# Kernel optimization log

Hardware: AMD Instinct MI355X
Metric: run time of the kernel (lower is better)

Reference implementation:

```python
import jax, jax.numpy as jnp
import numpy as np

B, IN_DIM, HID, N_WIRES = 8192, 2048, 2048, 8


def setup_inputs() -> dict:
    key = jax.random.key(0)
    ks = jax.random.split(key, 12)
    fan_in = IN_DIM + HID
    w_scale = 1.0 / np.sqrt(fan_in)  # ~ nn.Linear default init scale
    mk_w = lambda k: jax.random.normal(k, (N_WIRES, fan_in), jnp.float32) * w_scale
    mk_b = lambda k: jax.random.normal(k, (N_WIRES,), jnp.float32) * w_scale
    return {
        "x": jax.random.normal(ks[0], (B, IN_DIM), jnp.float32),
        "hx": jax.random.normal(ks[1], (B, HID), jnp.float32),
        "cx": jax.random.normal(ks[2], (B, HID), jnp.float32),
        "Wf": mk_w(ks[3]), "bf": mk_b(ks[4]),
        "Wi": mk_w(ks[5]), "bi": mk_b(ks[6]),
        "Wg": mk_w(ks[7]), "bg": mk_b(ks[8]),
        "Wo": mk_w(ks[9]), "bo": mk_b(ks[10]),
    }


def reference(x, hx, cx, Wf, bf, Wi, bi, Wg, bg, Wo, bo):
    combined = jnp.concatenate([x, hx], axis=1)  # [B, IN+HID]
    # Exact expectation of the RX-only circuit: E[#zeros - #ones] = sum_i cos(angle_i)
    q_exp = lambda W, b: jnp.sum(jnp.cos(combined @ W.T + b))
    f = jax.nn.sigmoid(q_exp(Wf, bf))
    i = jax.nn.sigmoid(q_exp(Wi, bi))
    g = jnp.tanh(q_exp(Wg, bg))
    o = jax.nn.sigmoid(q_exp(Wo, bo))
    cx_new = f * cx + i * g
    hx_new = o * jnp.tanh(cx_new)
    return hx_new, cx_new
```

## Files before the change

### kernel.cpp

```cpp
#include <hip/hip_runtime.h>
#include <hip/hip_bf16.h>
#include <cstdint>
#include <cstddef>

#define B_ROWS 8192
#define KDIM   4096
#define IN_DIM 2048
#define HIDDEN 2048
#define NJ     32
#define BK     64
#define SUBT   (KDIM / BK)
#define MROWS  16
#define TPB1   64
#define NBUF   4
#define GRID1  (B_ROWS / MROWS)

typedef __bf16 bf16x8 __attribute__((ext_vector_type(8)));
typedef float  f32x4  __attribute__((ext_vector_type(4)));

__device__ __forceinline__ bf16x8 cvt8(f32x4 a, f32x4 b) {
    bf16x8 r;
    r[0] = (__bf16)a.x; r[1] = (__bf16)a.y; r[2] = (__bf16)a.z; r[3] = (__bf16)a.w;
    r[4] = (__bf16)b.x; r[5] = (__bf16)b.y; r[6] = (__bf16)b.z; r[7] = (__bf16)b.w;
    return r;
}

__device__ __forceinline__ void gload_lds16(const void* g, void* lds) {
    __builtin_amdgcn_global_load_lds(
        (const __attribute__((address_space(1))) void*)g,
        (__attribute__((address_space(3))) void*)lds, 16, 0, 0);
}

extern "C" __global__ __launch_bounds__(TPB1)
void p1_full(const float* __restrict__ x,  const float* __restrict__ hx,
             const float* __restrict__ Wf, const float* __restrict__ Wi,
             const float* __restrict__ Wg, const float* __restrict__ Wo,
             const float* __restrict__ bfp, const float* __restrict__ bip,
             const float* __restrict__ bgp, const float* __restrict__ bop,
             float* __restrict__ qpart)
{
    __shared__ float Abuf[NBUF][MROWS * BK];
    __shared__ float Bbuf[NBUF][NJ * BK];

    const int lane = threadIdx.x & 63;
    const int lrow = lane & 15;
    const int rowblk = blockIdx.x * MROWS;

    const float* Ax = x  + (size_t)rowblk * IN_DIM;
    const float* Ah = hx + (size_t)rowblk * HIDDEN;

    int aOff[4];
#pragma unroll
    for (int p = 0; p < 4; ++p) {
        const int r  = p * 4 + (lane >> 4);
        const int cs = (lane & 15) ^ (r & 7);
        aOff[p] = r * 2048 + cs * 4;
    }
    const float* Wsrc[8] = {Wf, Wf, Wi, Wi, Wg, Wg, Wo, Wo};
    int bOffp[8];
#pragma unroll
    for (int sl = 0; sl < 8; ++sl) {
        const int j  = sl * 4 + (lane >> 4);
        const int j7 = j & 7;
        bOffp[sl] = j7 * KDIM + (((lane & 15) ^ j7) * 4);
    }

    int offA0[2], offA1[2], offB00[2], offB01[2], offB10[2], offB11[2];
#pragma unroll
    for (int st = 0; st < 2; ++st) {
        const int cu = st * 8 + (lane >> 4) * 2;
        offA0[st]  = lrow * 256 + (((cu + 0) ^ (lane & 7)) * 16);
        offA1[st]  = lrow * 256 + (((cu + 1) ^ (lane & 7)) * 16);
        offB00[st] = lrow * 256        + (((cu + 0) ^ (lane & 7)) * 16);
        offB01[st] = lrow * 256        + (((cu + 1) ^ (lane & 7)) * 16);
        offB10[st] = (lrow + 16) * 256 + (((cu + 0) ^ (lane & 7)) * 16);
        offB11[st] = (lrow + 16) * 256 + (((cu + 1) ^ (lane & 7)) * 16);
    }

    f32x4 acc0 = {0.f, 0.f, 0.f, 0.f};
    f32x4 acc1 = {0.f, 0.f, 0.f, 0.f};

    auto issue = [&](int s) {
        const int b = s & (NBUF - 1);
        const float* As = (s < SUBT / 2) ? (Ax + s * BK)
                                         : (Ah + (s - SUBT / 2) * BK);
#pragma unroll
        for (int p = 0; p < 4; ++p)
            gload_lds16(As + aOff[p], (char*)&Abuf[b][0] + p * 1024);
#pragma unroll
        for (int sl = 0; sl < 8; ++sl)
            gload_lds16(Wsrc[sl] + bOffp[sl] + s * BK,
                        (char*)&Bbuf[b][0] + sl * 1024);
    };
    auto compute = [&](int s) {
        const int b = s & (NBUF - 1);
        const char* Ab = (const char*)&Abuf[b][0];
        const char* Bb = (const char*)&Bbuf[b][0];
#pragma unroll
        for (int st = 0; st < 2; ++st) {
            f32x4 a0  = *reinterpret_cast<const f32x4*>(Ab + offA0[st]);
            f32x4 a1  = *reinterpret_cast<const f32x4*>(Ab + offA1[st]);
            f32x4 w00 = *reinterpret_cast<const f32x4*>(Bb + offB00[st]);
            f32x4 w01 = *reinterpret_cast<const f32x4*>(Bb + offB01[st]);
            f32x4 w10 = *reinterpret_cast<const f32x4*>(Bb + offB10[st]);
            f32x4 w11 = *reinterpret_cast<const f32x4*>(Bb + offB11[st]);
            bf16x8 af  = cvt8(a0, a1);
            bf16x8 bf0 = cvt8(w00, w01);
            bf16x8 bf1 = cvt8(w10, w11);
            acc0 = __builtin_amdgcn_mfma_f32_16x16x32_bf16(af, bf0, acc0, 0, 0, 0);
            acc1 = __builtin_amdgcn_mfma_f32_16x16x32_bf16(af, bf1, acc1, 0, 0, 0);
        }
    };

    issue(0);
    issue(1);
    issue(2);
#pragma unroll 4
    for (int s = 0; s < SUBT; ++s) {
        if (s + 3 < SUBT) issue(s + 3);
        if (s < SUBT - 3)
            asm volatile("s_waitcnt vmcnt(36)" ::: "memory");
        else if (s == SUBT - 3)
            asm volatile("s_waitcnt vmcnt(24)" ::: "memory");
        else if (s == SUBT - 2)
            asm volatile("s_waitcnt vmcnt(12)" ::: "memory");
        else
            asm volatile("s_waitcnt vmcnt(0)" ::: "memory");
        __builtin_amdgcn_sched_barrier(0);
        compute(s);
    }

    const float b0v = ((lrow & 8) ? bip : bfp)[lrow & 7];
    const float b1v = ((lrow & 8) ? bop : bgp)[lrow & 7];
    float v0 = 0.f, v1 = 0.f;
#pragma unroll
    for (int r = 0; r < 4; ++r) {
        v0 += cosf(acc0[r] + b0v);
        v1 += cosf(acc1[r] + b1v);
    }
    v0 += __shfl_xor(v0, 1, 64);  v1 += __shfl_xor(v1, 1, 64);
    v0 += __shfl_xor(v0, 2, 64);  v1 += __shfl_xor(v1, 2, 64);
    v0 += __shfl_xor(v0, 4, 64);  v1 += __shfl_xor(v1, 4, 64);
    v0 += __shfl_xor(v0, 16, 64); v1 += __shfl_xor(v1, 16, 64);
    v0 += __shfl_xor(v0, 32, 64); v1 += __shfl_xor(v1, 32, 64);
    if ((lane & 55) == 0) {
        const int gg = (lane >> 3) & 1;
        qpart[blockIdx.x * 4 + gg]     = v0;
        qpart[blockIdx.x * 4 + gg + 2] = v1;
    }
}

extern "C" __global__ __launch_bounds__(256)
void p3_elementwise(const float* __restrict__ cx, const float* __restrict__ qpart,
                    float* __restrict__ out)
{
    __shared__ float qs[4][4];
    const int tid  = threadIdx.x;
    const int wave = tid >> 6;
    const int lane = tid & 63;

    const f32x4* qp4 = (const f32x4*)qpart;
    f32x4 qa = qp4[tid];
    f32x4 qb = qp4[tid + 256];
    f32x4 qp = {qa.x + qb.x, qa.y + qb.y, qa.z + qb.z, qa.w + qb.w};
#pragma unroll
    for (int m = 1; m <= 32; m <<= 1) {
        qp.x += __shfl_xor(qp.x, m, 64);
        qp.y += __shfl_xor(qp.y, m, 64);
        qp.z += __shfl_xor(qp.z, m, 64);
        qp.w += __shfl_xor(qp.w, m, 64);
    }
    if (lane == 0) {
        qs[wave][0] = qp.x; qs[wave][1] = qp.y;
        qs[wave][2] = qp.z; qs[wave][3] = qp.w;
    }
    __syncthreads();
    const float qf = qs[0][0] + qs[1][0] + qs[2][0] + qs[3][0];
    const float qi = qs[0][1] + qs[1][1] + qs[2][1] + qs[3][1];
    const float qg = qs[0][2] + qs[1][2] + qs[2][2] + qs[3][2];
    const float qo = qs[0][3] + qs[1][3] + qs[2][3] + qs[3][3];

    const float f  = 1.f / (1.f + expf(-qf));
    const float ii = 1.f / (1.f + expf(-qi));
    const float g  = tanhf(qg);
    const float o  = 1.f / (1.f + expf(-qo));
    const float ig = ii * g;

    const size_t N  = (size_t)B_ROWS * HIDDEN;
    const size_t N4 = N >> 2;
    const f32x4* cx4 = (const f32x4*)cx;
    f32x4* outh = (f32x4*)out;
    f32x4* outc = (f32x4*)(out + N);

    for (size_t idx = (size_t)blockIdx.x * blockDim.x + tid; idx < N4;
         idx += (size_t)gridDim.x * blockDim.x) {
        f32x4 c = cx4[idx];
        f32x4 cn, hn;
        cn.x = fmaf(f, c.x, ig);
        cn.y = fmaf(f, c.y, ig);
        cn.z = fmaf(f, c.z, ig);
        cn.w = fmaf(f, c.w, ig);
        hn.x = o * tanhf(cn.x);
        hn.y = o * tanhf(cn.y);
        hn.z = o * tanhf(cn.z);
        hn.w = o * tanhf(cn.w);
        __builtin_nontemporal_store(cn, outc + idx);
        __builtin_nontemporal_store(hn, outh + idx);
    }
}

extern "C" void kernel_launch(void* const* d_in, const int* in_sizes, int n_in,
                              void* d_out, int out_size, void* d_ws, size_t ws_size,
                              hipStream_t stream)
{
    const float* x  = (const float*)d_in[0];
    const float* hx = (const float*)d_in[1];
    const float* cx = (const float*)d_in[2];
    const float* Wf = (const float*)d_in[3];
    const float* bf = (const float*)d_in[4];
    const float* Wi = (const float*)d_in[5];
    const float* bi = (const float*)d_in[6];
    const float* Wg = (const float*)d_in[7];
    const float* bg = (const float*)d_in[8];
    const float* Wo = (const float*)d_in[9];
    const float* bo = (const float*)d_in[10];
    float* out = (float*)d_out;

    float* qpart = (float*)d_ws;

    p1_full<<<dim3(GRID1), dim3(TPB1), 0, stream>>>(
        x, hx, Wf, Wi, Wg, Wo, bf, bi, bg, bo, qpart);
    p3_elementwise<<<dim3(2048), dim3(256), 0, stream>>>(cx, qpart, out);
}
```

Measured before the change: 64.93 us.

## Split K across two waves per block with LDS reduction of accumulators

```diff
diff --git a/kernel.cpp b/kernel.cpp
--- a/kernel.cpp
+++ b/kernel.cpp
@@ -9,10 +9,11 @@
 #define HIDDEN 2048
 #define NJ     32
 #define BK     64
-#define SUBT   (KDIM / BK)
+#define KHALF  2048
+#define SUBT   (KHALF / BK)
 #define MROWS  16
-#define TPB1   64
-#define NBUF   4
+#define TPB1   128
+#define NBUF   3
 #define GRID1  (B_ROWS / MROWS)
 
 typedef __bf16 bf16x8 __attribute__((ext_vector_type(8)));
@@ -39,15 +40,19 @@
              const float* __restrict__ bgp, const float* __restrict__ bop,
              float* __restrict__ qpart)
 {
-    __shared__ float Abuf[NBUF][MROWS * BK];
-    __shared__ float Bbuf[NBUF][NJ * BK];
-
-    const int lane = threadIdx.x & 63;
+    __shared__ float Abuf[2][NBUF][MROWS * BK];
+    __shared__ float Bbuf[2][NBUF][NJ * BK];
+
+    const int tid  = threadIdx.x;
+    const int wave = tid >> 6;
+    const int lane = tid & 63;
     const int lrow = lane & 15;
     const int rowblk = blockIdx.x * MROWS;
 
-    const float* Ax = x  + (size_t)rowblk * IN_DIM;
-    const float* Ah = hx + (size_t)rowblk * HIDDEN;
+    const float* Aglob = (wave == 0)
+        ? (x  + (size_t)rowblk * IN_DIM)
+        : (hx + (size_t)rowblk * HIDDEN);
+    const int kw = wave * KHALF;
 
     int aOff[4];
 #pragma unroll
@@ -81,21 +86,20 @@
     f32x4 acc1 = {0.f, 0.f, 0.f, 0.f};
 
     auto issue = [&](int s) {
-        const int b = s & (NBUF - 1);
-        const float* As = (s < SUBT / 2) ? (Ax + s * BK)
-                                         : (Ah + (s - SUBT / 2) * BK);
+        const int b = s % NBUF;
 #pragma unroll
         for (int p = 0; p < 4; ++p)
-            gload_lds16(As + aOff[p], (char*)&Abuf[b][0] + p * 1024);
+            gload_lds16(Aglob + aOff[p] + s * BK,
+                        (char*)&Abuf[wave][b][0] + p * 1024);
 #pragma unroll
         for (int sl = 0; sl < 8; ++sl)
-            gload_lds16(Wsrc[sl] + bOffp[sl] + s * BK,
-                        (char*)&Bbuf[b][0] + sl * 1024);
+            gload_lds16(Wsrc[sl] + bOffp[sl] + kw + s * BK,
+                        (char*)&Bbuf[wave][b][0] + sl * 1024);
     };
     auto compute = [&](int s) {
-        const int b = s & (NBUF - 1);
-        const char* Ab = (const char*)&Abuf[b][0];
-        const char* Bb = (const char*)&Bbuf[b][0];
+        const int b = s % NBUF;
+        const char* Ab = (const char*)&Abuf[wave][b][0];
+        const char* Bb = (const char*)&Bbuf[wave][b][0];
 #pragma unroll
         for (int st = 0; st < 2; ++st) {
             f32x4 a0  = *reinterpret_cast<const f32x4*>(Ab + offA0[st]);
@@ -114,39 +118,50 @@
 
     issue(0);
     issue(1);
-    issue(2);
-#pragma unroll 4
-    for (int s = 0; s < SUBT; ++s) {
-        if (s + 3 < SUBT) issue(s + 3);
-        if (s < SUBT - 3)
-            asm volatile("s_waitcnt vmcnt(36)" ::: "memory");
-        else if (s == SUBT - 3)
-            asm volatile("s_waitcnt vmcnt(24)" ::: "memory");
-        else if (s == SUBT - 2)
-            asm volatile("s_waitcnt vmcnt(12)" ::: "memory");
-        else
-            asm volatile("s_waitcnt vmcnt(0)" ::: "memory");
+    for (int s = 0; s < SUBT - 2; ++s) {
+        issue(s + 2);
+        asm volatile("s_waitcnt vmcnt(24)" ::: "memory");
         __builtin_amdgcn_sched_barrier(0);
         compute(s);
     }
-
-    const float b0v = ((lrow & 8) ? bip : bfp)[lrow & 7];
-    const float b1v = ((lrow & 8) ? bop : bgp)[lrow & 7];
-    float v0 = 0.f, v1 = 0.f;
-#pragma unroll
-    for (int r = 0; r < 4; ++r) {
-        v0 += cosf(acc0[r] + b0v);
-        v1 += cosf(acc1[r] + b1v);
-    }
-    v0 += __shfl_xor(v0, 1, 64);  v1 += __shfl_xor(v1, 1, 64);
-    v0 += __shfl_xor(v0, 2, 64);  v1 += __shfl_xor(v1, 2, 64);
-    v0 += __shfl_xor(v0, 4, 64);  v1 += __shfl_xor(v1, 4, 64);
-    v0 += __shfl_xor(v0, 16, 64); v1 += __shfl_xor(v1, 16, 64);
-    v0 += __shfl_xor(v0, 32, 64); v1 += __shfl_xor(v1, 32, 64);
-    if ((lane & 55) == 0) {
-        const int gg = (lane >> 3) & 1;
-        qpart[blockIdx.x * 4 + gg]     = v0;
-        qpart[blockIdx.x * 4 + gg + 2] = v1;
+    asm volatile("s_waitcnt vmcnt(12)" ::: "memory");
+    __builtin_amdgcn_sched_barrier(0);
+    compute(SUBT - 2);
+    asm volatile("s_waitcnt vmcnt(0)" ::: "memory");
+    __builtin_amdgcn_sched_barrier(0);
+    compute(SUBT - 1);
+
+    float* scratch = &Abuf[0][0][0];
+    __syncthreads();
+    if (wave == 1) {
+        f32x4* sp = reinterpret_cast<f32x4*>(scratch);
+        sp[lane * 2]     = acc0;
+        sp[lane * 2 + 1] = acc1;
+    }
+    __syncthreads();
+    if (wave == 0) {
+        const f32x4* sp = reinterpret_cast<const f32x4*>(scratch);
+        acc0 += sp[lane * 2];
+        acc1 += sp[lane * 2 + 1];
+
+        const float b0v = ((lrow & 8) ? bip : bfp)[lrow & 7];
+        const float b1v = ((lrow & 8) ? bop : bgp)[lrow & 7];
+        float v0 = 0.f, v1 = 0.f;
+#pragma unroll
+        for (int r = 0; r < 4; ++r) {
+            v0 += cosf(acc0[r] + b0v);
+            v1 += cosf(acc1[r] + b1v);
+        }
+        v0 += __shfl_xor(v0, 1, 64);  v1 += __shfl_xor(v1, 1, 64);
+        v0 += __shfl_xor(v0, 2, 64);  v1 += __shfl_xor(v1, 2, 64);
+        v0 += __shfl_xor(v0, 4, 64);  v1 += __shfl_xor(v1, 4, 64);
+        v0 += __shfl_xor(v0, 16, 64); v1 += __shfl_xor(v1, 16, 64);
+        v0 += __shfl_xor(v0, 32, 64); v1 += __shfl_xor(v1, 32, 64);
+        if ((lane & 55) == 0) {
+            const int gg = (lane >> 3) & 1;
+            qpart[blockIdx.x * 4 + gg]     = v0;
+            qpart[blockIdx.x * 4 + gg + 2] = v1;
+        }
     }
 }
 
```

New measurement: 64.73 us. Within noise of the previous version (-0.3%).
